# Performance work log

Hardware: AMD Instinct MI355X
Metric: run time of the kernel (lower is better)

Reference implementation:

```python
import jax, jax.numpy as jnp
import numpy as np


def setup_inputs() -> dict:
    key = jax.random.key(0)
    ks = jax.random.split(key, 7)
    B, D, N, R = 256, 5120, 16, 160  # batch, d_inner, d_state, dt_rank
    x = jax.random.normal(ks[0], (B, D), jnp.float32)
    h0 = jax.random.normal(ks[1], (B, D, N), jnp.float32)
    W_x_dt = jax.random.normal(ks[2], (D, R), jnp.float32) * (1.0 / np.sqrt(D))
    W_dt = jax.random.normal(ks[3], (R, D), jnp.float32) * (1.0 / np.sqrt(R))
    b_dt = jax.random.normal(ks[4], (D,), jnp.float32)
    W_BC = jax.random.normal(ks[5], (D, 2 * N), jnp.float32) * (1.0 / np.sqrt(D))
    A_log = jax.random.normal(ks[6], (D, N), jnp.float32)
    return {"x": x, "h0": h0, "W_x_dt": W_x_dt, "W_dt": W_dt,
            "b_dt": b_dt, "W_BC": W_BC, "A_log": A_log}


def reference(x, h0, W_x_dt, W_dt, b_dt, W_BC, A_log):
    # Single-token Mamba selective SSM step (batch dims squeezed: x [B,D], h0 [B,D,N]).
    N = A_log.shape[1]
    # delta_t = softplus(dt_proj(delta_t_proj(x)))  -> [B, D]
    dt = jax.nn.softplus((x @ W_x_dt) @ W_dt + b_dt)
    # BC projection, split into B and C parts -> [B, N] each
    BC = x @ W_BC
    Bm, Cm = BC[:, :N], BC[:, N:]
    A = -jnp.exp(A_log)                              # [D, N]
    delta_A = jnp.exp(A[None, :, :] * dt[:, :, None])   # [B, D, N]
    delta_Bx = (dt * x)[:, :, None] * Bm[:, None, :]     # [B, D, N]
    h = delta_A * h0 + delta_Bx                          # new hidden state
    # y = h @ C (per-batch bmm over state dim) + x residual
    y = jnp.einsum('bdn,bn->bd', h, Cm) + x              # [B, D]
    return y
```

## Files before the change

kernel.cpp:

```cpp
#include <hip/hip_runtime.h>
#include <math.h>

#define BB 256
#define DD 5120
#define NN 16
#define RR 160
#define CT 192
#define NSPLIT 32
#define TMP_ELEMS (BB * CT)
#define NEGA_ELEMS (DD * NN)

__global__ __launch_bounds__(256) void k1_gemm(const float* __restrict__ x,
                                               const float* __restrict__ Wxdt,
                                               const float* __restrict__ Wbc,
                                               float* __restrict__ part) {
    __shared__ float xs[32][68];
    __shared__ float ws[32][64];
    const int tid = threadIdx.x;
    const int tx = tid & 15, ty = tid >> 4;
    const int c0 = blockIdx.x * 64;
    const int b0 = blockIdx.y * 64;
    const int k0 = blockIdx.z * 160;
    float acc[4][4] = {};

    for (int kc = 0; kc < 160; kc += 32) {
        {
            const int i  = tid >> 3;
            const int j4 = (tid & 7) * 4;
            #pragma unroll
            for (int rep = 0; rep < 2; ++rep) {
                const int row = i + rep * 32;
                const float4 v = *(const float4*)&x[(size_t)(b0 + row) * DD + k0 + kc + j4];
                xs[j4 + 0][row] = v.x;
                xs[j4 + 1][row] = v.y;
                xs[j4 + 2][row] = v.z;
                xs[j4 + 3][row] = v.w;
            }
        }
        {
            const int c4 = (tid & 15) * 4;
            const int r0 = tid >> 4;
            #pragma unroll
            for (int rep = 0; rep < 2; ++rep) {
                const int r  = r0 + rep * 16;
                const int kg = k0 + kc + r;
                const int cg = c0 + c4;
                float4 v;
                if (cg < RR) v = *(const float4*)&Wxdt[(size_t)kg * RR + cg];
                else         v = *(const float4*)&Wbc[(size_t)kg * 32 + (cg - RR)];
                *(float4*)&ws[r][c4] = v;
            }
        }
        __syncthreads();
        #pragma unroll
        for (int k = 0; k < 32; ++k) {
            const float4 a4 = *(const float4*)&xs[k][ty * 4];
            const float4 w4 = *(const float4*)&ws[k][tx * 4];
            const float av[4] = {a4.x, a4.y, a4.z, a4.w};
            const float wv[4] = {w4.x, w4.y, w4.z, w4.w};
            #pragma unroll
            for (int u = 0; u < 4; ++u)
                #pragma unroll
                for (int v = 0; v < 4; ++v)
                    acc[u][v] = fmaf(av[u], wv[v], acc[u][v]);
        }
        __syncthreads();
    }

    float* p = part + (size_t)blockIdx.z * TMP_ELEMS;
    #pragma unroll
    for (int u = 0; u < 4; ++u) {
        const int b = b0 + ty * 4 + u;
        *(float4*)&p[b * CT + c0 + tx * 4] =
            make_float4(acc[u][0], acc[u][1], acc[u][2], acc[u][3]);
    }
}

__global__ __launch_bounds__(256) void k_red(const float* __restrict__ part,
                                             const float* __restrict__ Alog,
                                             float* __restrict__ tmp,
                                             float* __restrict__ negA) {
    const int idx = blockIdx.x * 256 + threadIdx.x;
    if (idx < TMP_ELEMS) {
        float s = 0.f;
        #pragma unroll
        for (int z = 0; z < NSPLIT; ++z) s += part[(size_t)z * TMP_ELEMS + idx];
        tmp[idx] = s;
    } else {
        const int j = idx - TMP_ELEMS;
        negA[j] = -__expf(Alog[j]);
    }
}

__global__ __launch_bounds__(256) void k23_fused(const float* __restrict__ x,
                                                 const float* __restrict__ h0,
                                                 const float* __restrict__ Wdt,
                                                 const float* __restrict__ bdt,
                                                 const float* __restrict__ tmp,
                                                 const float* __restrict__ negA,
                                                 float* __restrict__ out) {
    __shared__ float ts[32][34];
    __shared__ float ws[32][64];
    __shared__ float As[64][17];
    __shared__ float BCs[32][33];
    const int tid = threadIdx.x;
    const int tx = tid & 15, ty = tid >> 4;
    const int d0 = blockIdx.x * 64;
    const int b0 = blockIdx.y * 32;

    {
        const int i  = tid >> 2;
        const int n4 = (tid & 3) * 4;
        const float4 v = *(const float4*)&negA[(size_t)(d0 + i) * NN + n4];
        As[i][n4 + 0] = v.x; As[i][n4 + 1] = v.y;
        As[i][n4 + 2] = v.z; As[i][n4 + 3] = v.w;
    }
    {
        const int row = tid >> 3;
        const int c4  = (tid & 7) * 4;
        const float4 v = *(const float4*)&tmp[(size_t)(b0 + row) * CT + RR + c4];
        BCs[row][c4 + 0] = v.x; BCs[row][c4 + 1] = v.y;
        BCs[row][c4 + 2] = v.z; BCs[row][c4 + 3] = v.w;
    }

    float acc[2][4] = {};
    for (int kc = 0; kc < RR; kc += 32) {
        {
            const int row = tid >> 3;
            const int j4  = (tid & 7) * 4;
            const float4 v = *(const float4*)&tmp[(size_t)(b0 + row) * CT + kc + j4];
            ts[j4 + 0][row] = v.x;
            ts[j4 + 1][row] = v.y;
            ts[j4 + 2][row] = v.z;
            ts[j4 + 3][row] = v.w;
        }
        {
            const int c4 = (tid & 15) * 4;
            const int r0 = tid >> 4;
            #pragma unroll
            for (int rep = 0; rep < 2; ++rep) {
                const int r = r0 + rep * 16;
                *(float4*)&ws[r][c4] = *(const float4*)&Wdt[(size_t)(kc + r) * DD + d0 + c4];
            }
        }
        __syncthreads();
        #pragma unroll
        for (int k = 0; k < 32; ++k) {
            const float a0 = ts[k][ty * 2 + 0];
            const float a1 = ts[k][ty * 2 + 1];
            const float4 w4 = *(const float4*)&ws[k][tx * 4];
            const float wv[4] = {w4.x, w4.y, w4.z, w4.w};
            #pragma unroll
            for (int v = 0; v < 4; ++v) {
                acc[0][v] = fmaf(a0, wv[v], acc[0][v]);
                acc[1][v] = fmaf(a1, wv[v], acc[1][v]);
            }
        }
        __syncthreads();
    }

    const float4 bv = *(const float4*)&bdt[d0 + tx * 4];
    const float bb[4] = {bv.x, bv.y, bv.z, bv.w};

    #pragma unroll
    for (int u = 0; u < 2; ++u) {
        const int b = b0 + ty * 2 + u;
        const size_t base = (size_t)b * DD + d0 + tx * 4;
        const float4 xv = *(const float4*)&x[base];
        const float xs4[4] = {xv.x, xv.y, xv.z, xv.w};
        const float* bm = &BCs[ty * 2 + u][0];
        const float* cm = &BCs[ty * 2 + u][16];
        float y[4];
        #pragma unroll
        for (int v = 0; v < 4; ++v) {
            const int dsub = tx * 4 + v;
            const float z  = acc[u][v] + bb[v];
            const float dt = fmaxf(z, 0.f) + log1pf(__expf(-fabsf(z)));
            const float xe = xs4[v];
            const float dtx = dt * xe;
            const float* hp = &h0[(base + (size_t)v) * NN];
            float acc_y = xe;
            #pragma unroll
            for (int n4 = 0; n4 < NN; n4 += 4) {
                const float4 a4 = *(const float4*)&As[dsub][n4];
                const float4 h4 = *(const float4*)&hp[n4];
                const float av[4] = {a4.x, a4.y, a4.z, a4.w};
                const float hv[4] = {h4.x, h4.y, h4.z, h4.w};
                #pragma unroll
                for (int q = 0; q < 4; ++q) {
                    const int n = n4 + q;
                    const float dA = __expf(av[q] * dt);
                    const float h  = fmaf(dA, hv[q], dtx * bm[n]);
                    acc_y = fmaf(h, cm[n], acc_y);
                }
            }
            y[v] = acc_y;
        }
        *(float4*)&out[base] = make_float4(y[0], y[1], y[2], y[3]);
    }
}

extern "C" void kernel_launch(void* const* d_in, const int* in_sizes, int n_in,
                              void* d_out, int out_size, void* d_ws, size_t ws_size,
                              hipStream_t stream) {
    const float* x    = (const float*)d_in[0];
    const float* h0   = (const float*)d_in[1];
    const float* Wxdt = (const float*)d_in[2];
    const float* Wdt  = (const float*)d_in[3];
    const float* bdt  = (const float*)d_in[4];
    const float* Wbc  = (const float*)d_in[5];
    const float* Alog = (const float*)d_in[6];
    float* out = (float*)d_out;

    float* part = (float*)d_ws;
    float* tmp  = part + (size_t)NSPLIT * TMP_ELEMS;
    float* negA = tmp + TMP_ELEMS;

    k1_gemm<<<dim3(3, 4, NSPLIT), 256, 0, stream>>>(x, Wxdt, Wbc, part);
    k_red<<<dim3((TMP_ELEMS + NEGA_ELEMS) / 256), 256, 0, stream>>>(part, Alog, tmp, negA);
    k23_fused<<<dim3(DD / 64, BB / 32), 256, 0, stream>>>(x, h0, Wdt, bdt, tmp, negA, out);
}
```

Baseline: 185.8 us.

## Split fused dt GEMM and SSM epilogue into separate kernels

Breaks the fused dt-projection plus state-update kernel into two kernels. k_dt computes softplus(dt) and writes it to a workspace that reuses the partials buffer. k_epi then streams h0 with one thread per (b,d) cell, using four independent accumulators. This is meant to improve the h0 access pattern and occupancy for the bandwidth-bound epilogue. In exchange it adds an extra launch and a round trip of the B×D dt array through global memory.

Result: no change. 184.0 us (-0.9%).

```diff
diff --git a/kernel.cpp b/kernel.cpp
--- a/kernel.cpp
+++ b/kernel.cpp
@@ -92,36 +92,16 @@
     }
 }
 
-__global__ __launch_bounds__(256) void k23_fused(const float* __restrict__ x,
-                                                 const float* __restrict__ h0,
-                                                 const float* __restrict__ Wdt,
-                                                 const float* __restrict__ bdt,
-                                                 const float* __restrict__ tmp,
-                                                 const float* __restrict__ negA,
-                                                 float* __restrict__ out) {
+__global__ __launch_bounds__(256) void k_dt(const float* __restrict__ tmp,
+                                            const float* __restrict__ Wdt,
+                                            const float* __restrict__ bdt,
+                                            float* __restrict__ dtA) {
     __shared__ float ts[32][34];
     __shared__ float ws[32][64];
-    __shared__ float As[64][17];
-    __shared__ float BCs[32][33];
     const int tid = threadIdx.x;
     const int tx = tid & 15, ty = tid >> 4;
     const int d0 = blockIdx.x * 64;
     const int b0 = blockIdx.y * 32;
-
-    {
-        const int i  = tid >> 2;
-        const int n4 = (tid & 3) * 4;
-        const float4 v = *(const float4*)&negA[(size_t)(d0 + i) * NN + n4];
-        As[i][n4 + 0] = v.x; As[i][n4 + 1] = v.y;
-        As[i][n4 + 2] = v.z; As[i][n4 + 3] = v.w;
-    }
-    {
-        const int row = tid >> 3;
-        const int c4  = (tid & 7) * 4;
-        const float4 v = *(const float4*)&tmp[(size_t)(b0 + row) * CT + RR + c4];
-        BCs[row][c4 + 0] = v.x; BCs[row][c4 + 1] = v.y;
-        BCs[row][c4 + 2] = v.z; BCs[row][c4 + 3] = v.w;
-    }
 
     float acc[2][4] = {};
     for (int kc = 0; kc < RR; kc += 32) {
@@ -161,42 +141,58 @@
 
     const float4 bv = *(const float4*)&bdt[d0 + tx * 4];
     const float bb[4] = {bv.x, bv.y, bv.z, bv.w};
-
     #pragma unroll
     for (int u = 0; u < 2; ++u) {
         const int b = b0 + ty * 2 + u;
-        const size_t base = (size_t)b * DD + d0 + tx * 4;
-        const float4 xv = *(const float4*)&x[base];
-        const float xs4[4] = {xv.x, xv.y, xv.z, xv.w};
-        const float* bm = &BCs[ty * 2 + u][0];
-        const float* cm = &BCs[ty * 2 + u][16];
-        float y[4];
+        float4 o;
+        float* op = (float*)&o;
         #pragma unroll
         for (int v = 0; v < 4; ++v) {
-            const int dsub = tx * 4 + v;
-            const float z  = acc[u][v] + bb[v];
-            const float dt = fmaxf(z, 0.f) + log1pf(__expf(-fabsf(z)));
-            const float xe = xs4[v];
-            const float dtx = dt * xe;
-            const float* hp = &h0[(base + (size_t)v) * NN];
-            float acc_y = xe;
-            #pragma unroll
-            for (int n4 = 0; n4 < NN; n4 += 4) {
-                const float4 a4 = *(const float4*)&As[dsub][n4];
-                const float4 h4 = *(const float4*)&hp[n4];
-                const float av[4] = {a4.x, a4.y, a4.z, a4.w};
-                const float hv[4] = {h4.x, h4.y, h4.z, h4.w};
-                #pragma unroll
-                for (int q = 0; q < 4; ++q) {
-                    const int n = n4 + q;
-                    const float dA = __expf(av[q] * dt);
-                    const float h  = fmaf(dA, hv[q], dtx * bm[n]);
-                    acc_y = fmaf(h, cm[n], acc_y);
-                }
-            }
-            y[v] = acc_y;
-        }
-        *(float4*)&out[base] = make_float4(y[0], y[1], y[2], y[3]);
+            const float z = acc[u][v] + bb[v];
+            op[v] = fmaxf(z, 0.f) + log1pf(__expf(-fabsf(z)));
+        }
+        *(float4*)&dtA[(size_t)b * DD + d0 + tx * 4] = o;
+    }
+}
+
+__global__ __launch_bounds__(256) void k_epi(const float* __restrict__ x,
+                                             const float* __restrict__ h0,
+                                             const float* __restrict__ dtA,
+                                             const float* __restrict__ negA,
+                                             const float* __restrict__ tmp,
+                                             float* __restrict__ out) {
+    __shared__ float bc[32];
+    const int tid = threadIdx.x;
+    const int b  = blockIdx.y;
+    const int d0 = blockIdx.x * 512;
+    if (tid < 32) bc[tid] = tmp[(size_t)b * CT + RR + tid];
+    __syncthreads();
+
+    #pragma unroll
+    for (int r = 0; r < 2; ++r) {
+        const int d = d0 + r * 256 + tid;
+        const size_t cell = (size_t)b * DD + d;
+        const float dt  = dtA[cell];
+        const float xe  = x[cell];
+        const float dtx = dt * xe;
+        const float* hp = &h0[cell * NN];
+        const float* ap = &negA[(size_t)d * NN];
+        float acc4[4] = {xe, 0.f, 0.f, 0.f};
+        #pragma unroll
+        for (int n4 = 0; n4 < NN; n4 += 4) {
+            const float4 a4 = *(const float4*)&ap[n4];
+            const float4 h4 = *(const float4*)&hp[n4];
+            const float av[4] = {a4.x, a4.y, a4.z, a4.w};
+            const float hv[4] = {h4.x, h4.y, h4.z, h4.w};
+            #pragma unroll
+            for (int q = 0; q < 4; ++q) {
+                const int n = n4 + q;
+                const float dA = __expf(av[q] * dt);
+                const float h  = fmaf(dA, hv[q], dtx * bc[n]);
+                acc4[q] = fmaf(h, bc[16 + n], acc4[q]);
+            }
+        }
+        out[cell] = (acc4[0] + acc4[1]) + (acc4[2] + acc4[3]);
     }
 }
 
@@ -215,8 +211,10 @@
     float* part = (float*)d_ws;
     float* tmp  = part + (size_t)NSPLIT * TMP_ELEMS;
     float* negA = tmp + TMP_ELEMS;
+    float* dtA  = part;
 
     k1_gemm<<<dim3(3, 4, NSPLIT), 256, 0, stream>>>(x, Wxdt, Wbc, part);
     k_red<<<dim3((TMP_ELEMS + NEGA_ELEMS) / 256), 256, 0, stream>>>(part, Alog, tmp, negA);
-    k23_fused<<<dim3(DD / 64, BB / 32), 256, 0, stream>>>(x, h0, Wdt, bdt, tmp, negA, out);
-}
+    k_dt<<<dim3(DD / 64, BB / 32), 256, 0, stream>>>(tmp, Wdt, bdt, dtA);
+    k_epi<<<dim3(DD / 512, BB), 256, 0, stream>>>(x, h0, dtA, negA, tmp, out);
+}
```
